# Optimization experiments

Hardware: AMD Instinct MI355X
Metric: run time of the kernel (lower is better)

Reference implementation:

```python
import jax, jax.numpy as jnp
import numpy as np

IGNORE_INDEX = -100  # torch default; targets here are all valid but mask is honored
REDUCTION = "mean"

B, D, V = 4096, 2048, 32000


def setup_inputs() -> dict:
    key = jax.random.key(0)
    k1, k2, k3 = jax.random.split(key, 3)
    x = jax.random.normal(k1, (B, D), dtype=jnp.float32)
    # LM-head weight, scaled like typical init
    L = jax.random.normal(k2, (V, D), dtype=jnp.float32) * (1.0 / np.sqrt(D))
    target = jax.random.randint(k3, (B,), 0, V, dtype=jnp.int64)
    class_weight = jnp.ones((V,), dtype=jnp.float32)  # unnormalized per-class weight
    return {"x": x, "L": L, "target": target, "class_weight": class_weight}


def reference(x, L, target, class_weight):
    """Fused linear + weighted cross-entropy (reduction='mean', ignore_index=-100).

    Equivalent math to MyLinearCrossEntropyFunction: the torch code chunks over
    batches/classes/features with an online softmax solely to avoid materializing
    logits; the unchunked math is a single GEMM + stable log-softmax CE.
    """
    # logits: [B, V]
    logits = jnp.einsum("bd,vd->bv", x, L)
    logZ = jax.nn.logsumexp(logits, axis=1)                      # [B]
    valid = target != IGNORE_INDEX                               # [B] bool
    t_safe = jnp.where(valid, target, 0)
    gathered = jnp.take_along_axis(logits, t_safe[:, None], axis=1)[:, 0]  # [B]
    # effective per-sample weight: class weight of target, zeroed where ignored
    wt = jnp.where(valid, class_weight[t_safe], jnp.zeros((), logits.dtype))  # [B]
    per_sample = wt * (logZ - gathered)
    total = per_sample.sum()
    if REDUCTION == "mean":
        return total / wt.sum()
    return total
```

## Files before the change

kernel.cpp:

```cpp
#include <hip/hip_runtime.h>

#define B_ 4096
#define D_ 2048
#define V_ 32000

#define BM 256
#define BN 256
#define BKB 128
#define NT (D_ / BKB)
#define NCHUNK (V_ / 64)

typedef __attribute__((ext_vector_type(8))) int   int8v;
typedef __attribute__((ext_vector_type(4))) int   int4v;
typedef __attribute__((ext_vector_type(4))) float f32x4;

#define SCALE_A 127
#define SCALE_B 121

__device__ __forceinline__ void load_lds16(const void* g, void* l) {
    __builtin_amdgcn_global_load_lds(
        (const __attribute__((address_space(1))) void*)g,
        (__attribute__((address_space(3))) void*)l,
        16, 0, 0);
}

__device__ __forceinline__ int8v frag(const unsigned char* buf, int base, int p0, int p1) {
    union { int8v v8; int4v v4[2]; } u;
    u.v4[0] = *(const int4v*)(buf + base + p0);
    u.v4[1] = *(const int4v*)(buf + base + p1);
    return u.v8;
}

__global__ void cast_f32_to_fp8(const float* __restrict__ x,
                                const float* __restrict__ L,
                                unsigned int* __restrict__ xq,
                                unsigned int* __restrict__ Lq) {
    const int n4x = (B_ * D_) / 4;
    const int n4l = (V_ * D_) / 4;
    int i = blockIdx.x * blockDim.x + threadIdx.x;
    const float* in; unsigned int* out; float ps; int j;
    if (i < n4x) { in = x; out = xq; ps = 1.0f;  j = i; }
    else         { j = i - n4x; if (j >= n4l) return; in = L; out = Lq; ps = 64.0f; }
    float4 v = ((const float4*)in)[j];
    int w = __builtin_amdgcn_cvt_pk_fp8_f32(v.x * ps, v.y * ps, 0, false);
    w     = __builtin_amdgcn_cvt_pk_fp8_f32(v.z * ps, v.w * ps, w, true);
    out[j] = (unsigned)w;
}

__global__ __launch_bounds__(512, 2)
void gemm_ce_partials(const unsigned char* __restrict__ xq,
                      const unsigned char* __restrict__ Lq,
                      const int* __restrict__ targ,
                      float2* __restrict__ partials,
                      float* __restrict__ gathered) {
    __shared__ __align__(16) unsigned char As[2][BM * BKB];
    __shared__ __align__(16) unsigned char Bs[2][BN * BKB];

    const int tid    = threadIdx.x;
    const int lane   = tid & 63;
    const int wid    = tid >> 6;
    const int wave_m = wid >> 2;
    const int wave_n = wid & 3;
    const int quad   = lane >> 4;
    const int l16    = lane & 15;
    const int swz    = l16 & 7;

    const int m0 = blockIdx.x * BM;
    const int n0 = blockIdx.y * BN;

    const int r0 = tid >> 3;
    const int c0 = (tid & 7) ^ (r0 & 7);
    const unsigned char* sA = xq + (size_t)(m0 + r0) * D_ + c0 * 16;
    const unsigned char* sB = Lq + (size_t)(n0 + r0) * D_ + c0 * 16;
    const int d0 = tid * 16;
#define STEP (64 * D_)
#define DSTEP 8192

    f32x4 acc[8][4];
#pragma unroll
    for (int i = 0; i < 8; ++i)
#pragma unroll
        for (int j = 0; j < 4; ++j)
            acc[i][j] = (f32x4){0.f, 0.f, 0.f, 0.f};

    const int p0 = ((quad ^ swz) << 4);
    const int p1 = p0 ^ 64;

    const int arow = (wave_m * 128 + l16) * BKB;
    const int brow = (wave_n * 64 + l16) * BKB;
#define AB(mi) (arow + (mi) * (16 * BKB))
#define BB(ni) (brow + (ni) * (16 * BKB))
#define MM(A, B, MI, NI)                                                     \
    acc[MI][NI] = __builtin_amdgcn_mfma_scale_f32_16x16x128_f8f6f4(          \
        A, B, acc[MI][NI], 0, 0, 0, SCALE_A, 0, SCALE_B)

#pragma unroll
    for (int p = 0; p < 4; ++p) {
        load_lds16(sA + (size_t)p * STEP, &As[0][d0 + p * DSTEP]);
        load_lds16(sB + (size_t)p * STEP, &Bs[0][d0 + p * DSTEP]);
    }
    asm volatile("s_waitcnt vmcnt(0)" ::: "memory");
    __builtin_amdgcn_s_barrier();

    for (int kt = 0; kt < NT; ++kt) {
        const int cur = kt & 1;
        const int nxt = cur ^ 1;
        const size_t k1 = (size_t)(kt + 1) * BKB;
        const bool pf = (kt + 1 < NT);
        const unsigned char* Ac = As[cur];
        const unsigned char* Bc = Bs[cur];

        int8v a0, a1, a2, a3, b0, b1, b2, b3, s;

        a0 = frag(Ac, AB(0), p0, p1);
        a1 = frag(Ac, AB(1), p0, p1);
        b0 = frag(Bc, BB(0), p0, p1);
        a2 = frag(Ac, AB(2), p0, p1);
        a3 = frag(Ac, AB(3), p0, p1);
        b1 = frag(Bc, BB(1), p0, p1);
        if (pf) {
            load_lds16(sB + k1, &Bs[nxt][d0]);
            load_lds16(sB + k1 + (size_t)STEP, &Bs[nxt][d0 + DSTEP]);
        }
        __builtin_amdgcn_s_barrier();
        __builtin_amdgcn_s_setprio(1);
        MM(a0, b0, 0, 0); MM(a1, b0, 1, 0);
        __builtin_amdgcn_s_setprio(0);

        b2 = frag(Bc, BB(2), p0, p1);
        b3 = frag(Bc, BB(3), p0, p1);
        s  = frag(Ac, AB(4), p0, p1);
        if (pf) {
            load_lds16(sB + k1 + (size_t)2 * STEP, &Bs[nxt][d0 + 2 * DSTEP]);
            load_lds16(sB + k1 + (size_t)3 * STEP, &Bs[nxt][d0 + 3 * DSTEP]);
        }
        __builtin_amdgcn_s_barrier();
        __builtin_amdgcn_s_setprio(1);
        MM(a2, b0, 2, 0); MM(a3, b0, 3, 0);
        MM(a0, b1, 0, 1); MM(a1, b1, 1, 1); MM(a2, b1, 2, 1); MM(a3, b1, 3, 1);
        __builtin_amdgcn_s_setprio(0);

        if (pf) {
            load_lds16(sA + k1, &As[nxt][d0]);
            load_lds16(sA + k1 + (size_t)STEP, &As[nxt][d0 + DSTEP]);
        }
        __builtin_amdgcn_s_barrier();
        __builtin_amdgcn_s_setprio(1);
        MM(a0, b2, 0, 2); MM(a1, b2, 1, 2); MM(a2, b2, 2, 2); MM(a3, b2, 3, 2);
        MM(a0, b3, 0, 3); MM(a1, b3, 1, 3); MM(a2, b3, 2, 3); MM(a3, b3, 3, 3);
        __builtin_amdgcn_s_setprio(0);

        a0 = frag(Ac, AB(5), p0, p1);
        a1 = frag(Ac, AB(6), p0, p1);
        a2 = frag(Ac, AB(7), p0, p1);
        if (pf) {
            load_lds16(sA + k1 + (size_t)2 * STEP, &As[nxt][d0 + 2 * DSTEP]);
            load_lds16(sA + k1 + (size_t)3 * STEP, &As[nxt][d0 + 3 * DSTEP]);
        }
        __builtin_amdgcn_s_barrier();
        __builtin_amdgcn_s_setprio(1);
        MM(s, b0, 4, 0); MM(s, b1, 4, 1); MM(s, b2, 4, 2); MM(s, b3, 4, 3);
        MM(a0, b0, 5, 0); MM(a0, b1, 5, 1); MM(a0, b2, 5, 2); MM(a0, b3, 5, 3);
        MM(a1, b0, 6, 0); MM(a1, b1, 6, 1); MM(a1, b2, 6, 2); MM(a1, b3, 6, 3);
        MM(a2, b0, 7, 0); MM(a2, b1, 7, 1); MM(a2, b2, 7, 2); MM(a2, b3, 7, 3);
        __builtin_amdgcn_s_setprio(0);
        asm volatile("s_waitcnt vmcnt(0)" ::: "memory");
        __builtin_amdgcn_s_barrier();
    }

    const int row_base = m0 + wave_m * 128;
    const int col_base = n0 + wave_n * 64;
    const int chunk    = blockIdx.y * 4 + wave_n;

    int tv[32];
#pragma unroll
    for (int mi = 0; mi < 8; ++mi)
#pragma unroll
        for (int r = 0; r < 4; ++r)
            tv[mi * 4 + r] = targ[row_base + mi * 16 + quad * 4 + r];

    float M = acc[0][0][0];
#pragma unroll
    for (int mi = 0; mi < 8; ++mi)
#pragma unroll
        for (int ni = 0; ni < 4; ++ni)
#pragma unroll
            for (int r = 0; r < 4; ++r)
                M = fmaxf(M, acc[mi][ni][r]);
#pragma unroll
    for (int off = 1; off < 64; off <<= 1)
        M = fmaxf(M, __shfl_xor(M, off, 64));

    float sv[32];
#pragma unroll
    for (int mi = 0; mi < 8; ++mi)
#pragma unroll
        for (int r = 0; r < 4; ++r)
            sv[mi * 4 + r] = __expf(acc[mi][0][r] - M) + __expf(acc[mi][1][r] - M) +
                             __expf(acc[mi][2][r] - M) + __expf(acc[mi][3][r] - M);
#pragma unroll
    for (int off = 1; off < 16; off <<= 1)
#pragma unroll
        for (int i = 0; i < 32; ++i)
            sv[i] += __shfl_xor(sv[i], off, 64);

    if (l16 == 0) {
#pragma unroll
        for (int mi = 0; mi < 8; ++mi)
#pragma unroll
            for (int r = 0; r < 4; ++r) {
                int row = row_base + mi * 16 + quad * 4 + r;
                partials[(size_t)row * NCHUNK + chunk] = make_float2(M, sv[mi * 4 + r]);
            }
    }

#pragma unroll
    for (int mi = 0; mi < 8; ++mi)
#pragma unroll
        for (int r = 0; r < 4; ++r) {
            int row = row_base + mi * 16 + quad * 4 + r;
            int cb  = col_base + l16;
            int t   = tv[mi * 4 + r];
            if (cb      == t) gathered[row] = acc[mi][0][r];
            if (cb + 16 == t) gathered[row] = acc[mi][1][r];
            if (cb + 32 == t) gathered[row] = acc[mi][2][r];
            if (cb + 48 == t) gathered[row] = acc[mi][3][r];
        }
}

__global__ void combine_rows(const float2* __restrict__ partials,
                             const float* __restrict__ gathered,
                             const int* __restrict__ targ,
                             const float* __restrict__ cw,
                             float* __restrict__ row_loss,
                             float* __restrict__ row_w) {
    int row  = blockIdx.x * 4 + (threadIdx.x >> 6);
    int lane = threadIdx.x & 63;
    float m = -3.0e38f, s = 0.f;
    for (int c = lane; c < NCHUNK; c += 64) {
        float2 p = partials[(size_t)row * NCHUNK + c];
        float nm = fmaxf(m, p.x);
        s = s * __expf(m - nm) + p.y * __expf(p.x - nm);
        m = nm;
    }
#pragma unroll
    for (int off = 32; off; off >>= 1) {
        float om = __shfl_xor(m, off, 64);
        float os = __shfl_xor(s, off, 64);
        float nm = fmaxf(m, om);
        s = s * __expf(m - nm) + os * __expf(om - nm);
        m = nm;
    }
    if (lane == 0) {
        float logZ = m + __logf(s);
        int t = targ[row];
        bool valid = (t != -100);
        int ts = valid ? t : 0;
        float w = valid ? cw[ts] : 0.f;
        row_loss[row] = w * (logZ - gathered[row]);
        row_w[row]    = w;
    }
}

__global__ void final_reduce(const float* __restrict__ rl,
                             const float* __restrict__ rw,
                             float* __restrict__ out) {
    __shared__ float sl[4], sw[4];
    float a = 0.f, b = 0.f;
    for (int i = threadIdx.x; i < B_; i += 256) { a += rl[i]; b += rw[i]; }
#pragma unroll
    for (int off = 32; off; off >>= 1) {
        a += __shfl_xor(a, off, 64);
        b += __shfl_xor(b, off, 64);
    }
    int w = threadIdx.x >> 6;
    if ((threadIdx.x & 63) == 0) { sl[w] = a; sw[w] = b; }
    __syncthreads();
    if (threadIdx.x == 0) {
        float ta = sl[0] + sl[1] + sl[2] + sl[3];
        float tb = sw[0] + sw[1] + sw[2] + sw[3];
        out[0] = ta / tb;
    }
}

extern "C" void kernel_launch(void* const* d_in, const int* in_sizes, int n_in,
                              void* d_out, int out_size, void* d_ws, size_t ws_size,
                              hipStream_t stream) {
    const float* x  = (const float*)d_in[0];
    const float* L  = (const float*)d_in[1];
    const int* targ = (const int*)d_in[2];
    const float* cw = (const float*)d_in[3];
    float* out = (float*)d_out;

    char* ws = (char*)d_ws;
    size_t o = 0;
    unsigned char* xq = (unsigned char*)(ws + o);  o += (size_t)B_ * D_;
    unsigned char* Lq = (unsigned char*)(ws + o);  o += (size_t)V_ * D_;
    float2* partials = (float2*)(ws + o);          o += (size_t)B_ * NCHUNK * 8;
    float* gathered = (float*)(ws + o);            o += (size_t)B_ * 4;
    float* row_loss = (float*)(ws + o);            o += (size_t)B_ * 4;
    float* row_w    = (float*)(ws + o);            o += (size_t)B_ * 4;
    (void)ws_size;

    {
        int n4 = (B_ * D_) / 4 + (V_ * D_) / 4;
        cast_f32_to_fp8<<<(n4 + 255) / 256, 256, 0, stream>>>(
            x, L, (unsigned*)xq, (unsigned*)Lq);
    }

    {
        dim3 grid(B_ / BM, V_ / BN);
        gemm_ce_partials<<<grid, 512, 0, stream>>>(xq, Lq, targ, partials, gathered);
    }

    combine_rows<<<B_ / 4, 256, 0, stream>>>(partials, gathered, targ, cw, row_loss, row_w);

    final_reduce<<<1, 256, 0, stream>>>(row_loss, row_w, out);
}
```

Baseline: 650.2 us.

## Load A fragments directly from global memory and grid-stride the fp8 cast

The GEMM kernel stops staging the x (A) tile in LDS and has each wave read its A fragments straight from global memory into registers, keeping only B double-buffered in LDS. The four intra-iteration barriers collapse to one per k-step, and the MFMA schedule becomes two blocks of 16. This halves LDS use, which could raise occupancy or cut barrier cost, but it relies on global/L2 latency for A, with no prefetch ahead of use. The cast kernel also becomes a grid-stride loop with a fixed 4096-block grid.

```diff
diff --git a/kernel.cpp b/kernel.cpp
--- a/kernel.cpp
+++ b/kernel.cpp
@@ -28,6 +28,13 @@
     union { int8v v8; int4v v4[2]; } u;
     u.v4[0] = *(const int4v*)(buf + base + p0);
     u.v4[1] = *(const int4v*)(buf + base + p1);
+    return u.v8;
+}
+
+__device__ __forceinline__ int8v gfrag(const unsigned char* p) {
+    union { int8v v8; int4v v4[2]; } u;
+    u.v4[0] = *(const int4v*)(p);
+    u.v4[1] = *(const int4v*)(p + 64);
     return u.v8;
 }
 
@@ -37,14 +44,17 @@
                                 unsigned int* __restrict__ Lq) {
     const int n4x = (B_ * D_) / 4;
     const int n4l = (V_ * D_) / 4;
-    int i = blockIdx.x * blockDim.x + threadIdx.x;
-    const float* in; unsigned int* out; float ps; int j;
-    if (i < n4x) { in = x; out = xq; ps = 1.0f;  j = i; }
-    else         { j = i - n4x; if (j >= n4l) return; in = L; out = Lq; ps = 64.0f; }
-    float4 v = ((const float4*)in)[j];
-    int w = __builtin_amdgcn_cvt_pk_fp8_f32(v.x * ps, v.y * ps, 0, false);
-    w     = __builtin_amdgcn_cvt_pk_fp8_f32(v.z * ps, v.w * ps, w, true);
-    out[j] = (unsigned)w;
+    const int total = n4x + n4l;
+    const int stride = gridDim.x * blockDim.x;
+    for (int i = blockIdx.x * blockDim.x + threadIdx.x; i < total; i += stride) {
+        const float* in; unsigned int* out; float ps; int j;
+        if (i < n4x) { in = x; out = xq; ps = 1.0f;  j = i; }
+        else         { in = L; out = Lq; ps = 64.0f; j = i - n4x; }
+        float4 v = ((const float4*)in)[j];
+        int w = __builtin_amdgcn_cvt_pk_fp8_f32(v.x * ps, v.y * ps, 0, false);
+        w     = __builtin_amdgcn_cvt_pk_fp8_f32(v.z * ps, v.w * ps, w, true);
+        out[j] = (unsigned)w;
+    }
 }
 
 __global__ __launch_bounds__(512, 2)
@@ -53,7 +63,6 @@
                       const int* __restrict__ targ,
                       float2* __restrict__ partials,
                       float* __restrict__ gathered) {
-    __shared__ __align__(16) unsigned char As[2][BM * BKB];
     __shared__ __align__(16) unsigned char Bs[2][BN * BKB];
 
     const int tid    = threadIdx.x;
@@ -70,12 +79,15 @@
 
     const int r0 = tid >> 3;
     const int c0 = (tid & 7) ^ (r0 & 7);
-    const unsigned char* sA = xq + (size_t)(m0 + r0) * D_ + c0 * 16;
     const unsigned char* sB = Lq + (size_t)(n0 + r0) * D_ + c0 * 16;
     const int d0 = tid * 16;
 #define STEP (64 * D_)
 #define DSTEP 8192
 
+    const unsigned char* pA =
+        xq + (size_t)(m0 + wave_m * 128 + l16) * D_ + (quad << 4);
+#define AOFF(mi) ((size_t)(mi) * 16 * D_)
+
     f32x4 acc[8][4];
 #pragma unroll
     for (int i = 0; i < 8; ++i)
@@ -86,84 +98,61 @@
     const int p0 = ((quad ^ swz) << 4);
     const int p1 = p0 ^ 64;
 
-    const int arow = (wave_m * 128 + l16) * BKB;
     const int brow = (wave_n * 64 + l16) * BKB;
-#define AB(mi) (arow + (mi) * (16 * BKB))
 #define BB(ni) (brow + (ni) * (16 * BKB))
 #define MM(A, B, MI, NI)                                                     \
     acc[MI][NI] = __builtin_amdgcn_mfma_scale_f32_16x16x128_f8f6f4(          \
         A, B, acc[MI][NI], 0, 0, 0, SCALE_A, 0, SCALE_B)
 
 #pragma unroll
-    for (int p = 0; p < 4; ++p) {
-        load_lds16(sA + (size_t)p * STEP, &As[0][d0 + p * DSTEP]);
+    for (int p = 0; p < 4; ++p)
         load_lds16(sB + (size_t)p * STEP, &Bs[0][d0 + p * DSTEP]);
-    }
     asm volatile("s_waitcnt vmcnt(0)" ::: "memory");
     __builtin_amdgcn_s_barrier();
 
     for (int kt = 0; kt < NT; ++kt) {
         const int cur = kt & 1;
         const int nxt = cur ^ 1;
-        const size_t k1 = (size_t)(kt + 1) * BKB;
+        const size_t kk = (size_t)kt * BKB;
+        const size_t k1 = kk + BKB;
         const bool pf = (kt + 1 < NT);
-        const unsigned char* Ac = As[cur];
         const unsigned char* Bc = Bs[cur];
 
-        int8v a0, a1, a2, a3, b0, b1, b2, b3, s;
-
-        a0 = frag(Ac, AB(0), p0, p1);
-        a1 = frag(Ac, AB(1), p0, p1);
-        b0 = frag(Bc, BB(0), p0, p1);
-        a2 = frag(Ac, AB(2), p0, p1);
-        a3 = frag(Ac, AB(3), p0, p1);
-        b1 = frag(Bc, BB(1), p0, p1);
+        int8v b0 = frag(Bc, BB(0), p0, p1);
+        int8v b1 = frag(Bc, BB(1), p0, p1);
+        int8v b2 = frag(Bc, BB(2), p0, p1);
+        int8v b3 = frag(Bc, BB(3), p0, p1);
+
         if (pf) {
-            load_lds16(sB + k1, &Bs[nxt][d0]);
-            load_lds16(sB + k1 + (size_t)STEP, &Bs[nxt][d0 + DSTEP]);
+#pragma unroll
+            for (int p = 0; p < 4; ++p)
+                load_lds16(sB + k1 + (size_t)p * STEP, &Bs[nxt][d0 + p * DSTEP]);
         }
-        __builtin_amdgcn_s_barrier();
+
+        int8v a0 = gfrag(pA + kk + AOFF(0));
+        int8v a1 = gfrag(pA + kk + AOFF(1));
+        int8v a2 = gfrag(pA + kk + AOFF(2));
+        int8v a3 = gfrag(pA + kk + AOFF(3));
+
         __builtin_amdgcn_s_setprio(1);
-        MM(a0, b0, 0, 0); MM(a1, b0, 1, 0);
+        MM(a0, b0, 0, 0); MM(a0, b1, 0, 1); MM(a0, b2, 0, 2); MM(a0, b3, 0, 3);
+        MM(a1, b0, 1, 0); MM(a1, b1, 1, 1); MM(a1, b2, 1, 2); MM(a1, b3, 1, 3);
+        MM(a2, b0, 2, 0); MM(a2, b1, 2, 1); MM(a2, b2, 2, 2); MM(a2, b3, 2, 3);
+        MM(a3, b0, 3, 0); MM(a3, b1, 3, 1); MM(a3, b2, 3, 2); MM(a3, b3, 3, 3);
         __builtin_amdgcn_s_setprio(0);
 
-        b2 = frag(Bc, BB(2), p0, p1);
-        b3 = frag(Bc, BB(3), p0, p1);
-        s  = frag(Ac, AB(4), p0, p1);
-        if (pf) {
-            load_lds16(sB + k1 + (size_t)2 * STEP, &Bs[nxt][d0 + 2 * DSTEP]);
-            load_lds16(sB + k1 + (size_t)3 * STEP, &Bs[nxt][d0 + 3 * DSTEP]);
-        }
-        __builtin_amdgcn_s_barrier();
+        int8v a4 = gfrag(pA + kk + AOFF(4));
+        int8v a5 = gfrag(pA + kk + AOFF(5));
+        int8v a6 = gfrag(pA + kk + AOFF(6));
+        int8v a7 = gfrag(pA + kk + AOFF(7));
+
         __builtin_amdgcn_s_setprio(1);
-        MM(a2, b0, 2, 0); MM(a3, b0, 3, 0);
-        MM(a0, b1, 0, 1); MM(a1, b1, 1, 1); MM(a2, b1, 2, 1); MM(a3, b1, 3, 1);
+        MM(a4, b0, 4, 0); MM(a4, b1, 4, 1); MM(a4, b2, 4, 2); MM(a4, b3, 4, 3);
+        MM(a5, b0, 5, 0); MM(a5, b1, 5, 1); MM(a5, b2, 5, 2); MM(a5, b3, 5, 3);
+        MM(a6, b0, 6, 0); MM(a6, b1, 6, 1); MM(a6, b2, 6, 2); MM(a6, b3, 6, 3);
+        MM(a7, b0, 7, 0); MM(a7, b1, 7, 1); MM(a7, b2, 7, 2); MM(a7, b3, 7, 3);
         __builtin_amdgcn_s_setprio(0);
 
-        if (pf) {
-            load_lds16(sA + k1, &As[nxt][d0]);
-            load_lds16(sA + k1 + (size_t)STEP, &As[nxt][d0 + DSTEP]);
-        }
-        __builtin_amdgcn_s_barrier();
-        __builtin_amdgcn_s_setprio(1);
-        MM(a0, b2, 0, 2); MM(a1, b2, 1, 2); MM(a2, b2, 2, 2); MM(a3, b2, 3, 2);
-        MM(a0, b3, 0, 3); MM(a1, b3, 1, 3); MM(a2, b3, 2, 3); MM(a3, b3, 3, 3);
-        __builtin_amdgcn_s_setprio(0);
-
-        a0 = frag(Ac, AB(5), p0, p1);
-        a1 = frag(Ac, AB(6), p0, p1);
-        a2 = frag(Ac, AB(7), p0, p1);
-        if (pf) {
-            load_lds16(sA + k1 + (size_t)2 * STEP, &As[nxt][d0 + 2 * DSTEP]);
-            load_lds16(sA + k1 + (size_t)3 * STEP, &As[nxt][d0 + 3 * DSTEP]);
-        }
-        __builtin_amdgcn_s_barrier();
-        __builtin_amdgcn_s_setprio(1);
-        MM(s, b0, 4, 0); MM(s, b1, 4, 1); MM(s, b2, 4, 2); MM(s, b3, 4, 3);
-        MM(a0, b0, 5, 0); MM(a0, b1, 5, 1); MM(a0, b2, 5, 2); MM(a0, b3, 5, 3);
-        MM(a1, b0, 6, 0); MM(a1, b1, 6, 1); MM(a1, b2, 6, 2); MM(a1, b3, 6, 3);
-        MM(a2, b0, 7, 0); MM(a2, b1, 7, 1); MM(a2, b2, 7, 2); MM(a2, b3, 7, 3);
-        __builtin_amdgcn_s_setprio(0);
         asm volatile("s_waitcnt vmcnt(0)" ::: "memory");
         __builtin_amdgcn_s_barrier();
     }
@@ -302,11 +291,7 @@
     float* row_w    = (float*)(ws + o);            o += (size_t)B_ * 4;
     (void)ws_size;
 
-    {
-        int n4 = (B_ * D_) / 4 + (V_ * D_) / 4;
-        cast_f32_to_fp8<<<(n4 + 255) / 256, 256, 0, stream>>>(
-            x, L, (unsigned*)xq, (unsigned*)Lq);
-    }
+    cast_f32_to_fp8<<<4096, 256, 0, stream>>>(x, L, (unsigned*)xq, (unsigned*)Lq);
 
     {
         dim3 grid(B_ / BM, V_ / BN);
```

Result: slower. 975.2 us (+50.0%).
